# Performance work log

Measured on AMD Instinct MI355X. Metric: run time of the kernel, lower is better.

Reference implementation:

```python
import jax, jax.numpy as jnp
import numpy as np

BOX_WARP = 1.2
BMIN, BMAX = -0.6, 0.6   # sampler bbox
EPS_FD = 0.01            # finite-difference eps for SDF normals
RADIUS = 0.5             # sphere sdf bias radius
INV_S = 80.0             # sdf -> density sharpness (softplus clamp mode)
S_PER_RAY = 96


def _grid_sample_one(feat, uv):
    # feat: [C,H,W]; uv: [M,2] in [-1,1]; bilinear, align_corners=False, zeros padding
    C, H, W = feat.shape
    x = ((uv[:, 0] + 1.0) * W - 1.0) * 0.5
    y = ((uv[:, 1] + 1.0) * H - 1.0) * 0.5
    x0 = jnp.floor(x).astype(jnp.int32)
    y0 = jnp.floor(y).astype(jnp.int32)
    wx = x - x0
    wy = y - y0

    def g(ix, iy):
        valid = ((ix >= 0) & (ix < W) & (iy >= 0) & (iy < H)).astype(feat.dtype)
        v = feat[:, jnp.clip(iy, 0, H - 1), jnp.clip(ix, 0, W - 1)]  # [C,M]
        return v * valid[None, :]

    out = (g(x0, y0) * (1 - wx) * (1 - wy) + g(x0 + 1, y0) * wx * (1 - wy)
           + g(x0, y0 + 1) * (1 - wx) * wy + g(x0 + 1, y0 + 1) * wx * wy)
    return out.T  # [M,C]


def sample_from_planes(planes, coords):
    # planes: [N,3,C,H,W]; coords: [N,M,3] -> [N,M,3*C]
    N, P, C, H, W = planes.shape
    M = coords.shape[1]
    nc = coords * (2.0 / BOX_WARP)
    proj = jnp.stack([nc[..., (0, 1)], nc[..., (0, 2)], nc[..., (1, 2)]], axis=1)  # [N,3,M,2]
    s = jax.vmap(_grid_sample_one)(planes.reshape(N * P, C, H, W), proj.reshape(N * P, M, 2))
    return s.reshape(N, P, M, C).transpose(0, 2, 1, 3).reshape(N, M, P * C)


def decode(planes, coords, W1, b1, W2, b2):
    x = sample_from_planes(planes, coords)
    return jax.nn.relu(x @ W1 + b1) @ W2 + b2  # [N,M,4]


def render(planes, ro, rd, W1, b1, W2, b2):
    N, R, _ = ro.shape
    S = S_PER_RAY
    safe_rd = jnp.where(jnp.abs(rd) < 1e-9, 1e-9, rd)
    t1 = (BMIN - ro) / safe_rd
    t2 = (BMAX - ro) / safe_rd
    tn = jnp.maximum(jnp.max(jnp.minimum(t1, t2), axis=-1), 0.0)   # [N,R] ray_start (auto box)
    tf = jnp.min(jnp.maximum(t1, t2), axis=-1)                      # [N,R] ray_end
    span = jnp.maximum(tf - tn, 0.0)
    frac = (jnp.arange(S, dtype=ro.dtype) + 0.5) / S
    depths = tn[..., None] + span[..., None] * frac                 # [N,R,S]
    pts = (ro[:, :, None, :] + depths[..., None] * rd[:, :, None, :]).reshape(N, R * S, 3)

    x = decode(planes, pts, W1, b1, W2, b2)
    sdf = x[..., 0:1]
    rgb = jax.nn.sigmoid(x[..., 1:]) * (1 + 2 * 0.001) - 0.001

    # finite-difference SDF gradient (3 extra decoder passes)
    eye = jnp.eye(3, dtype=pts.dtype) * EPS_FD
    sdf_off = jnp.stack(
        [decode(planes, jnp.clip(pts + eye[i], BMIN, BMAX), W1, b1, W2, b2)[..., 0] for i in range(3)],
        axis=-1)                                                    # [N,M,3]
    sdf_grad = (sdf_off - sdf) / EPS_FD
    normal = sdf_grad / (jnp.linalg.norm(sdf_grad, axis=-1, keepdims=True) + 1e-8)

    # sphere sdf bias, sdf -> density, alpha compositing
    shifted = sdf[..., 0] + (jnp.linalg.norm(pts, axis=-1) - RADIUS)
    sigma = jax.nn.softplus(-shifted * INV_S).reshape(N, R, S)
    delta = (span / S)[..., None]
    alpha = 1.0 - jnp.exp(-sigma * delta)
    T = jnp.cumprod(1.0 - alpha + 1e-10, axis=-1)
    T = jnp.concatenate([jnp.ones_like(T[..., :1]), T[..., :-1]], axis=-1)
    w = alpha * T                                                   # [N,R,S]

    rgb_s = (w[..., None] * rgb.reshape(N, R, S, 3)).sum(-2)
    wsum = w.sum(-1, keepdims=True)
    rgb_s = rgb_s + (1.0 - wsum)                                    # white background
    depth_s = (w * depths).sum(-1, keepdims=True)
    normal_s = (w[..., None] * normal.reshape(N, R, S, 3)).sum(-2)
    return rgb_s, depth_s, wsum, sdf_grad, normal_s


def reference(planes, ray_origins, ray_directions, W1, b1, W2, b2, render_size):
    N = planes.shape[0]
    rgb_s, depth_s, wsum, sdf_grad, normal_s = render(planes, ray_origins, ray_directions, W1, b1, W2, b2)
    n = normal_s / (jnp.linalg.norm(normal_s, axis=-1, keepdims=True) + 1e-8)
    n = (n + 1.0) * 0.5
    n = n * wsum  # lerp(0, n, opacity)
    H = W = render_size
    comp_rgb = rgb_s.transpose(0, 2, 1).reshape(N, 3, H, W)
    comp_depth = depth_s.transpose(0, 2, 1).reshape(N, 1, H, W)
    opacity = wsum.transpose(0, 2, 1).reshape(N, 1, H, W)
    comp_normal = n.transpose(0, 2, 1).reshape(N, 3, H, W)
    return (comp_rgb, comp_depth, opacity, comp_normal, sdf_grad)


def setup_inputs():
    key = jax.random.key(0)
    k0, k1, k2 = jax.random.split(key, 3)
    N, C, Hp, rs = 1, 80, 64, 64
    planes = jax.random.normal(k0, (N, 3, C, Hp, Hp), jnp.float32)
    u = jnp.linspace(-0.45, 0.45, rs)
    uu, vv = jnp.meshgrid(u, u, indexing='xy')
    d = jnp.stack([uu, vv, -jnp.ones_like(uu)], -1).reshape(-1, 3)
    d = d / jnp.linalg.norm(d, axis=-1, keepdims=True)
    ray_directions = jnp.broadcast_to(d, (N, rs * rs, 3)).astype(jnp.float32)
    ray_origins = jnp.broadcast_to(jnp.array([0.0, 0.0, 1.5], jnp.float32), (N, rs * rs, 3))
    W1 = jax.random.normal(k1, (3 * C, 64), jnp.float32) * 0.05
    b1 = jnp.zeros((64,), jnp.float32)
    W2 = jax.random.normal(k2, (64, 4), jnp.float32) * 0.05
    b2 = jnp.zeros((4,), jnp.float32)
    return {"planes": planes, "ray_origins": ray_origins, "ray_directions": ray_directions,
            "W1": W1, "b1": b1, "W2": W2, "b2": b2, "render_size": rs}
```

## Files before the change

### kernel.cpp

```cpp
#include <hip/hip_runtime.h>
#include <hip/hip_bf16.h>
#include <hip/hip_fp16.h>

#define NUM_RAYS 4096
#define S_PER 96
#define NPTS (NUM_RAYS * S_PER)
#define CCH 80
#define HID 64

#define WSB_W2     256
#define WSB_B1     1536
#define WSB_B2     1856
#define WSB_W1S    4096
#define WSB_PT     40960



typedef __attribute__((ext_vector_type(8))) _Float16 half8;
typedef __attribute__((ext_vector_type(4))) float f32x4;

__device__ __forceinline__ float bf2f(__hip_bfloat16 v) { return __bfloat162float(v); }

__device__ __forceinline__ short f2hs(float f) {
  __half h = __float2half(f);
  short s; __builtin_memcpy(&s, &h, 2); return s;
}

template <bool BF16>
__device__ __forceinline__ float ldin(const void* p, size_t i) {
  if (BF16) return bf2f(((const __hip_bfloat16*)p)[i]);
  else      return ((const float*)p)[i];
}
template <bool BF16>
__device__ __forceinline__ void stout(void* p, size_t i, float v) {
  if (BF16) ((__hip_bfloat16*)p)[i] = __float2bfloat16(v);
  else      ((float*)p)[i] = v;
}

__device__ __forceinline__ __half2 h2cast(unsigned u) {
  __half2 r; __builtin_memcpy(&r, &u, 4); return r;
}

__device__ __forceinline__ bool detect_bf16(const void* rdv) {
  int lane = threadIdx.x & 63;
  const __hip_bfloat16* p = (const __hip_bfloat16*)rdv;
  float x = bf2f(p[lane * 3 + 0]);
  float y = bf2f(p[lane * 3 + 1]);
  float z = bf2f(p[lane * 3 + 2]);
  float n2 = x * x + y * y + z * z;
  bool ok = (n2 > 0.95f) && (n2 < 1.05f);
  return __ballot(ok) == ~0ull;
}

template <bool BF16>
__device__ __forceinline__ void prep_body(const void* __restrict__ W1,
                                          const void* __restrict__ b1,
                                          const void* __restrict__ W2,
                                          const void* __restrict__ b2,
                                          float* __restrict__ ws, int tid) {
  unsigned short* w1sw = (unsigned short*)((char*)ws + WSB_W1S);
  if (tid < 15360) {
    int p = tid / 5120;
    int r = tid - p * 5120;
    int ch, n;
    if (r < 4096) {
      int ccl  = r >> 11;
      int r2   = r & 2047;
      int j    = r2 & 7;
      int lane = (r2 >> 3) & 63;
      int nb   = r2 >> 9;
      ch = ccl * 32 + 8 * (lane >> 4) + j;
      n  = nb * 16 + (lane & 15);
    } else {
      int r2   = r - 4096;
      int j    = r2 & 7;
      int l31  = (r2 >> 3) & 31;
      int nb   = r2 >> 8;
      ch = 64 + 8 * (l31 >> 4) + j;
      n  = nb * 16 + (l31 & 15);
    }
    w1sw[tid] = (unsigned short)f2hs(ldin<BF16>(W1, (size_t)(p * 80 + ch) * 64 + n));
  }
  float* w2f = (float*)((char*)ws + WSB_W2);
  float* b1f = (float*)((char*)ws + WSB_B1);
  float* b2f = (float*)((char*)ws + WSB_B2);
  if (tid < 256) w2f[tid] = ldin<BF16>(W2, tid);
  if (tid < 64)  b1f[tid] = ldin<BF16>(b1, tid);
  if (tid < 4)   b2f[tid] = ldin<BF16>(b2, tid);
}

template <bool BF16>
__device__ __forceinline__ void transpose_body(const void* __restrict__ planes,
                                               float* __restrict__ ws) {
  int b  = blockIdx.x;
  int tt = b & 15;
  int ct = (b >> 4) % 5;
  int p  = b / 80;
  int tex = tt * 256 + threadIdx.x;
  unsigned u[8];
  #pragma unroll
  for (int i = 0; i < 8; i++) {
    int c0 = ct * 16 + 2 * i;
    float v0 = ldin<BF16>(planes, ((size_t)(p * 80 + c0) * 4096) + tex);
    float v1 = ldin<BF16>(planes, ((size_t)(p * 80 + c0 + 1) * 4096) + tex);
    unsigned s0 = (unsigned short)f2hs(v0);
    unsigned s1 = (unsigned short)f2hs(v1);
    u[i] = s0 | (s1 << 16);
  }
  unsigned short* ptb = (unsigned short*)((char*)ws + WSB_PT);
  uint4* dst = (uint4*)(ptb + ((size_t)(p * 4096 + tex) * 80 + ct * 16));
  dst[0] = make_uint4(u[0], u[1], u[2], u[3]);
  dst[1] = make_uint4(u[4], u[5], u[6], u[7]);
}

__global__ void setup_kernel(const void* __restrict__ planes,
                             const void* __restrict__ W1,
                             const void* __restrict__ b1,
                             const void* __restrict__ W2,
                             const void* __restrict__ b2,
                             const void* __restrict__ rd,
                             float* __restrict__ ws) {
  bool bf = detect_bf16(rd);
  if (blockIdx.x < 240) {
    if (bf) transpose_body<true >(planes, ws);
    else    transpose_body<false>(planes, ws);
  } else {
    int tid = (blockIdx.x - 240) * 256 + threadIdx.x;
    if (bf) prep_body<true >(W1, b1, W2, b2, ws, tid);
    else    prep_body<false>(W1, b1, W2, b2, ws, tid);
  }
}

struct TapInfo {
  float w00, w10, w01, w11;
  int o00, o10, o01, o11;
};
__device__ __forceinline__ TapInfo tap_setup(float u, float v) {
  TapInfo t;
  float fx = u * 32.0f + 31.5f;
  float fy = v * 32.0f + 31.5f;
  float flx = floorf(fx), fly = floorf(fy);
  int x0 = (int)flx, y0 = (int)fly;
  float wx = fx - flx, wy = fy - fly;
  int x1 = x0 + 1, y1 = y0 + 1;
  bool vx0 = (x0 >= 0) && (x0 < 64);
  bool vx1 = (x1 >= 0) && (x1 < 64);
  bool vy0 = (y0 >= 0) && (y0 < 64);
  bool vy1 = (y1 >= 0) && (y1 < 64);
  int cx0 = min(max(x0, 0), 63), cx1 = min(max(x1, 0), 63);
  int cy0 = min(max(y0, 0), 63), cy1 = min(max(y1, 0), 63);
  t.w00 = (1.0f - wx) * (1.0f - wy) * ((vx0 && vy0) ? 1.0f : 0.0f);
  t.w10 = wx * (1.0f - wy)          * ((vx1 && vy0) ? 1.0f : 0.0f);
  t.w01 = (1.0f - wx) * wy          * ((vx0 && vy1) ? 1.0f : 0.0f);
  t.w11 = wx * wy                   * ((vx1 && vy1) ? 1.0f : 0.0f);
  t.o00 = cy0 * 64 + cx0; t.o10 = cy0 * 64 + cx1;
  t.o01 = cy1 * 64 + cx0; t.o11 = cy1 * 64 + cx1;
  return t;
}

template <bool BF16>
__device__ __forceinline__ void fused_body(const void* __restrict__ ro,
                                           const void* __restrict__ rd,
                                           const float* __restrict__ ws,
                                           void* __restrict__ out,
                                           unsigned short* __restrict__ w1s,
                                           float* __restrict__ rec_v0,
                                           __half (*__restrict__ rec_h)[6],
                                           float* __restrict__ xfer,
                                           float (*__restrict__ red)[8]) {
  const unsigned short* ptb = (const unsigned short*)((const char*)ws + WSB_PT);
  const float* w2f = (const float*)((const char*)ws + WSB_W2);
  const float* b1f = (const float*)((const char*)ws + WSB_B1);
  const float* b2f = (const float*)((const char*)ws + WSB_B2);

  int tid = threadIdx.x;
  int wave = tid >> 6;
  int lane = tid & 63;
  int lane15 = lane & 15;
  int quad = lane >> 4;
  int ray = blockIdx.x;

  {
    const uint4* src = (const uint4*)((const char*)ws + WSB_W1S);
    uint4* dst = (uint4*)w1s;
    #pragma unroll
    for (int t = 0; t < 8; t++) {
      int idx = tid + 256 * t;
      if (idx < 1920) dst[idx] = src[idx];
    }
  }
  float4 w2reg[4];
  #pragma unroll
  for (int nb = 0; nb < 4; nb++)
    w2reg[nb] = *(const float4*)(w2f + (nb * 16 + lane15) * 4);

  float ox = ldin<BF16>(ro, (size_t)ray*3+0), oy = ldin<BF16>(ro, (size_t)ray*3+1), oz = ldin<BF16>(ro, (size_t)ray*3+2);
  float dx = ldin<BF16>(rd, (size_t)ray*3+0), dy = ldin<BF16>(rd, (size_t)ray*3+1), dz = ldin<BF16>(rd, (size_t)ray*3+2);
  float o3[3] = {ox, oy, oz}, d3[3] = {dx, dy, dz};
  float tmin = -1e30f, tmax = 1e30f;
  #pragma unroll
  for (int k = 0; k < 3; k++) {
    float sd = (fabsf(d3[k]) < 1e-9f) ? 1e-9f : d3[k];
    float ta = (-0.6f - o3[k]) / sd;
    float tb = ( 0.6f - o3[k]) / sd;
    tmin = fmaxf(tmin, fminf(ta, tb));
    tmax = fminf(tmax, fmaxf(ta, tb));
  }
  float tn = fmaxf(tmin, 0.0f);
  float span = fmaxf(tmax - tn, 0.0f);
  float delta = span * (1.0f / (float)S_PER);
  float b1x[4];
  #pragma unroll
  for (int nb = 0; nb < 4; nb++) b1x[nb] = b1f[nb * 16 + lane15];

  __syncthreads();

  #pragma unroll 1
  for (int it = 0; it < 6; it++) {
    int sbase = it * 16 + wave * 4;

    int sF = sbase + (lane15 >> 2);
    int d  = lane15 & 3;
    float depF = tn + span * (((float)sF + 0.5f) * (1.0f / (float)S_PER));
    float px = ox + depF * dx, py = oy + depF * dy, pz = oz + depF * dz;
    if (d == 1) px += 0.01f;
    if (d == 2) py += 0.01f;
    if (d == 3) pz += 0.01f;
    if (d > 0) {
      px = fminf(fmaxf(px, -0.6f), 0.6f);
      py = fminf(fmaxf(py, -0.6f), 0.6f);
      pz = fminf(fmaxf(pz, -0.6f), 0.6f);
    }
    const float inv = 1.0f / 0.6f;
    float ux = px * inv, uy = py * inv, uz = pz * inv;

    f32x4 acc[4];
    #pragma unroll
    for (int nb = 0; nb < 4; nb++) acc[nb] = (f32x4){0.f, 0.f, 0.f, 0.f};

    #pragma unroll 1
    for (int p = 0; p < 3; p++) {
      float u = (p == 2) ? uy : ux;
      float v = (p == 0) ? uy : uz;
      TapInfo t = tap_setup(u, v);
      __half2 hw00 = __float2half2_rn(t.w00);
      __half2 hw10 = __float2half2_rn(t.w10);
      __half2 hw01 = __float2half2_rn(t.w01);
      __half2 hw11 = __float2half2_rn(t.w11);
      const unsigned short* c00p = ptb + (size_t)p * 327680 + t.o00 * 80 + 8 * quad;
      const unsigned short* c10p = ptb + (size_t)p * 327680 + t.o10 * 80 + 8 * quad;
      const unsigned short* c01p = ptb + (size_t)p * 327680 + t.o01 * 80 + 8 * quad;
      const unsigned short* c11p = ptb + (size_t)p * 327680 + t.o11 * 80 + 8 * quad;
      const unsigned short* w1p = w1s + p * 5120;
      #pragma unroll
      for (int ccl = 0; ccl < 3; ccl++) {
        int4 afi = {0, 0, 0, 0};
        if (ccl < 2 || quad < 2) {
          uint4 q00 = *(const uint4*)(c00p + 32 * ccl);
          uint4 q10 = *(const uint4*)(c10p + 32 * ccl);
          uint4 q01 = *(const uint4*)(c01p + 32 * ccl);
          uint4 q11 = *(const uint4*)(c11p + 32 * ccl);
          unsigned u00[4] = {q00.x, q00.y, q00.z, q00.w};
          unsigned u10[4] = {q10.x, q10.y, q10.z, q10.w};
          unsigned u01[4] = {q01.x, q01.y, q01.z, q01.w};
          unsigned u11[4] = {q11.x, q11.y, q11.z, q11.w};
          int ae[4];
          #pragma unroll
          for (int q = 0; q < 4; q++) {
            __half2 f = __hmul2(h2cast(u00[q]), hw00);
            f = __hfma2(h2cast(u10[q]), hw10, f);
            f = __hfma2(h2cast(u01[q]), hw01, f);
            f = __hfma2(h2cast(u11[q]), hw11, f);
            int fi; __builtin_memcpy(&fi, &f, 4);
            ae[q] = fi;
          }
          afi.x = ae[0]; afi.y = ae[1]; afi.z = ae[2]; afi.w = ae[3];
        }
        half8 afr;
        __builtin_memcpy(&afr, &afi, 16);
        #pragma unroll
        for (int nb = 0; nb < 4; nb++) {
          int boff = (ccl < 2) ? (ccl * 2048 + (nb * 64 + lane) * 8)
                               : (4096 + (nb * 32 + (lane & 31)) * 8);
          half8 bfr = *(const half8*)(w1p + boff);
          acc[nb] = __builtin_amdgcn_mfma_f32_16x16x32_f16(afr, bfr, acc[nb], 0, 0, 0);
        }
      }
    }

    float vals[7];
    #pragma unroll
    for (int k = 0; k < 7; k++) vals[k] = 0.0f;
    #pragma unroll
    for (int nb = 0; nb < 4; nb++) {
      float4 w2r = w2reg[nb];
      float hr0 = fmaxf(acc[nb][0] + b1x[nb], 0.0f);
      vals[0] = fmaf(hr0, w2r.x, vals[0]);
      vals[4] = fmaf(hr0, w2r.y, vals[4]);
      vals[5] = fmaf(hr0, w2r.z, vals[5]);
      vals[6] = fmaf(hr0, w2r.w, vals[6]);
      float hr1 = fmaxf(acc[nb][1] + b1x[nb], 0.0f);
      float hr2 = fmaxf(acc[nb][2] + b1x[nb], 0.0f);
      float hr3 = fmaxf(acc[nb][3] + b1x[nb], 0.0f);
      vals[1] = fmaf(hr1, w2r.x, vals[1]);
      vals[2] = fmaf(hr2, w2r.x, vals[2]);
      vals[3] = fmaf(hr3, w2r.x, vals[3]);
    }
    #pragma unroll
    for (int mask = 1; mask < 16; mask <<= 1) {
      #pragma unroll
      for (int k = 0; k < 7; k++) vals[k] += __shfl_xor(vals[k], mask, 64);
    }

    if (lane15 == 0) {
      int sE = sbase + quad;
      rec_v0[sE] = vals[0];
      rec_h[sE][0] = __float2half(vals[1] - vals[0]);
      rec_h[sE][1] = __float2half(vals[2] - vals[0]);
      rec_h[sE][2] = __float2half(vals[3] - vals[0]);
      rec_h[sE][3] = __float2half(vals[4]);
      rec_h[sE][4] = __float2half(vals[5]);
      rec_h[sE][5] = __float2half(vals[6]);
    }
  }

  __syncthreads();

  float b2_0 = b2f[0], b2_1 = b2f[1], b2_2 = b2f[2], b2_3 = b2f[3];
  float a = 0.f, l = 0.f, pcr = 0.f, pcg = 0.f, pcb = 0.f, pnx = 0.f, pny = 0.f, pnz = 0.f, pdt = 0.f;
  if (tid < S_PER) {
    float v0 = rec_v0[tid];
    float d1 = __half2float(rec_h[tid][0]);
    float d2 = __half2float(rec_h[tid][1]);
    float d3 = __half2float(rec_h[tid][2]);
    float v4 = __half2float(rec_h[tid][3]);
    float v5 = __half2float(rec_h[tid][4]);
    float v6 = __half2float(rec_h[tid][5]);
    float sdf0 = v0 + b2_0;
    float g0 = d1 * 100.0f;
    float g1 = d2 * 100.0f;
    float g2 = d3 * 100.0f;
    size_t gid = (size_t)ray * S_PER + tid;
    stout<BF16>(out, (size_t)32768 + gid * 3 + 0, g0);
    stout<BF16>(out, (size_t)32768 + gid * 3 + 1, g1);
    stout<BF16>(out, (size_t)32768 + gid * 3 + 2, g2);
    pcr = 1.0f / (1.0f + expf(-(v4 + b2_1))) * 1.002f - 0.001f;
    pcg = 1.0f / (1.0f + expf(-(v5 + b2_2))) * 1.002f - 0.001f;
    pcb = 1.0f / (1.0f + expf(-(v6 + b2_3))) * 1.002f - 0.001f;
    pdt = tn + span * (((float)tid + 0.5f) * (1.0f / (float)S_PER));
    float ex = ox + pdt * dx, ey = oy + pdt * dy, ez = oz + pdt * dz;
    float pn = sqrtf(ex * ex + ey * ey + ez * ez);
    float shifted = sdf0 + pn - 0.5f;
    float xarg = -shifted * 80.0f;
    float sigma = (xarg > 20.0f) ? xarg : log1pf(expf(xarg));
    a = 1.0f - expf(-sigma * delta);
    float gl = sqrtf(g0 * g0 + g1 * g1 + g2 * g2) + 1e-8f;
    float igl = 1.0f / gl;
    pnx = g0 * igl; pny = g1 * igl; pnz = g2 * igl;
    l = logf(1.0f - a + 1e-10f);
  }

  float lv = l;
  #pragma unroll
  for (int off = 1; off < 64; off <<= 1) {
    float up = __shfl_up(lv, off, 64);
    if (lane >= off) lv += up;
  }
  if (tid == 63) xfer[0] = lv;
  __syncthreads();
  if (tid >= 64 && tid < S_PER) lv += xfer[0];

  float T = expf(lv - l);
  float w = (tid < S_PER) ? a * T : 0.0f;
  float q[8];
  q[0] = w;
  q[1] = w * pcr; q[2] = w * pcg; q[3] = w * pcb;
  q[4] = w * pnx; q[5] = w * pny; q[6] = w * pnz;
  q[7] = w * pdt;
  #pragma unroll
  for (int off = 1; off < 64; off <<= 1) {
    #pragma unroll
    for (int k = 0; k < 8; k++) q[k] += __shfl_xor(q[k], off, 64);
  }
  if (lane == 0) {
    #pragma unroll
    for (int k = 0; k < 8; k++) red[wave][k] = q[k];
  }
  __syncthreads();
  if (tid == 0) {
    float R[8];
    #pragma unroll
    for (int k = 0; k < 8; k++) R[k] = red[0][k] + red[1][k] + red[2][k] + red[3][k];
    float wsum = R[0];
    float nl = sqrtf(R[4] * R[4] + R[5] * R[5] + R[6] * R[6]) + 1e-8f;
    float inl = 1.0f / nl;
    float nrm3[3] = {R[4], R[5], R[6]};
    float rgb3[3] = {R[1], R[2], R[3]};
    #pragma unroll
    for (int c = 0; c < 3; c++) {
      float n = (nrm3[c] * inl + 1.0f) * 0.5f * wsum;
      stout<BF16>(out, (size_t)(c * 4096 + ray), rgb3[c] + 1.0f - wsum);
      stout<BF16>(out, (size_t)(20480 + c * 4096 + ray), n);
    }
    stout<BF16>(out, (size_t)(12288 + ray), R[7]);
    stout<BF16>(out, (size_t)(16384 + ray), wsum);
  }
}

__global__ __launch_bounds__(256) void fused_kernel(
    const void* __restrict__ ro,
    const void* __restrict__ rd,
    const float* __restrict__ ws,
    void* __restrict__ out) {
  __shared__ __align__(16) unsigned short w1s[15360];
  __shared__ float rec_v0[S_PER];
  __shared__ __half rec_h[S_PER][6];
  __shared__ float xfer[1];
  __shared__ float red[4][8];

  if (detect_bf16(rd)) fused_body<true >(ro, rd, ws, out, w1s, rec_v0, rec_h, xfer, red);
  else                 fused_body<false>(ro, rd, ws, out, w1s, rec_v0, rec_h, xfer, red);
}

extern "C" void kernel_launch(void* const* d_in, const int* in_sizes, int n_in,
                              void* d_out, int out_size, void* d_ws, size_t ws_size,
                              hipStream_t stream) {
  const void* planes = d_in[0];
  const void* ro     = d_in[1];
  const void* rd     = d_in[2];
  const void* W1     = d_in[3];
  const void* b1     = d_in[4];
  const void* W2     = d_in[5];
  const void* b2     = d_in[6];
  float* ws = (float*)d_ws;

  setup_kernel<<<304, 256, 0, stream>>>(planes, W1, b1, W2, b2, rd, ws);
  fused_kernel<<<NUM_RAYS, 256, 0, stream>>>(ro, rd, ws, d_out);
}
```

Measured before the change: 247.3 us.

## Unroll plane loop with double-buffered tap loads, DPP row reductions, W2 in LDS

Fully unrolls the three-plane loop and precomputes all bilinear tap offsets and weights up front. The four-corner feature loads for the next chunk are issued while the current chunk is blended and fed to MFMA, using two alternating register buffers. The goal is to hide global/L2 gather latency behind the f16 blending and matrix math. The 16-lane reduction now uses DPP row rotations instead of shfl_xor, and W2 moves from per-thread registers to shared memory to offset the extra registers the pipeline holds. The added live registers could lower occupancy.

```diff
diff --git a/kernel.cpp b/kernel.cpp
--- a/kernel.cpp
+++ b/kernel.cpp
@@ -40,6 +40,13 @@
 __device__ __forceinline__ __half2 h2cast(unsigned u) {
   __half2 r; __builtin_memcpy(&r, &u, 4); return r;
 }
+
+#define DPP_ADD(V, CTRL)                                                     \
+  do {                                                                       \
+    int s_ = __float_as_int(V);                                              \
+    int t_ = __builtin_amdgcn_update_dpp(0, s_, (CTRL), 0xF, 0xF, true);     \
+    V += __int_as_float(t_);                                                 \
+  } while (0)
 
 __device__ __forceinline__ bool detect_bf16(const void* rdv) {
   int lane = threadIdx.x & 63;
@@ -164,6 +171,7 @@
                                            const float* __restrict__ ws,
                                            void* __restrict__ out,
                                            unsigned short* __restrict__ w1s,
+                                           float* __restrict__ w2s,
                                            float* __restrict__ rec_v0,
                                            __half (*__restrict__ rec_h)[6],
                                            float* __restrict__ xfer,
@@ -189,10 +197,7 @@
       if (idx < 1920) dst[idx] = src[idx];
     }
   }
-  float4 w2reg[4];
-  #pragma unroll
-  for (int nb = 0; nb < 4; nb++)
-    w2reg[nb] = *(const float4*)(w2f + (nb * 16 + lane15) * 4);
+  w2s[tid] = w2f[tid];
 
   float ox = ldin<BF16>(ro, (size_t)ray*3+0), oy = ldin<BF16>(ro, (size_t)ray*3+1), oz = ldin<BF16>(ro, (size_t)ray*3+2);
   float dx = ldin<BF16>(rd, (size_t)ray*3+0), dy = ldin<BF16>(rd, (size_t)ray*3+1), dz = ldin<BF16>(rd, (size_t)ray*3+2);
@@ -215,6 +220,8 @@
 
   __syncthreads();
 
+  const char* pb = (const char*)ptb + 16 * quad;
+
   #pragma unroll 1
   for (int it = 0; it < 6; it++) {
     int sbase = it * 16 + wave * 4;
@@ -234,66 +241,94 @@
     const float inv = 1.0f / 0.6f;
     float ux = px * inv, uy = py * inv, uz = pz * inv;
 
+    TapInfo t0 = tap_setup(ux, uy);
+    TapInfo t1 = tap_setup(ux, uz);
+    TapInfo t2 = tap_setup(uy, uz);
+    unsigned f000 = (unsigned)(t0.o00 * 160);
+    unsigned f010 = (unsigned)(t0.o10 * 160);
+    unsigned f001 = (unsigned)(t0.o01 * 160);
+    unsigned f011 = (unsigned)(t0.o11 * 160);
+    unsigned f100 = (unsigned)(t1.o00 * 160) + 655360u;
+    unsigned f110 = (unsigned)(t1.o10 * 160) + 655360u;
+    unsigned f101 = (unsigned)(t1.o01 * 160) + 655360u;
+    unsigned f111 = (unsigned)(t1.o11 * 160) + 655360u;
+    unsigned f200 = (unsigned)(t2.o00 * 160) + 1310720u;
+    unsigned f210 = (unsigned)(t2.o10 * 160) + 1310720u;
+    unsigned f201 = (unsigned)(t2.o01 * 160) + 1310720u;
+    unsigned f211 = (unsigned)(t2.o11 * 160) + 1310720u;
+    __half2 h000 = __float2half2_rn(t0.w00), h010 = __float2half2_rn(t0.w10);
+    __half2 h001 = __float2half2_rn(t0.w01), h011 = __float2half2_rn(t0.w11);
+    __half2 h100 = __float2half2_rn(t1.w00), h110 = __float2half2_rn(t1.w10);
+    __half2 h101 = __float2half2_rn(t1.w01), h111 = __float2half2_rn(t1.w11);
+    __half2 h200 = __float2half2_rn(t2.w00), h210 = __float2half2_rn(t2.w10);
+    __half2 h201 = __float2half2_rn(t2.w01), h211 = __float2half2_rn(t2.w11);
+
     f32x4 acc[4];
     #pragma unroll
     for (int nb = 0; nb < 4; nb++) acc[nb] = (f32x4){0.f, 0.f, 0.f, 0.f};
 
-    #pragma unroll 1
-    for (int p = 0; p < 3; p++) {
-      float u = (p == 2) ? uy : ux;
-      float v = (p == 0) ? uy : uz;
-      TapInfo t = tap_setup(u, v);
-      __half2 hw00 = __float2half2_rn(t.w00);
-      __half2 hw10 = __float2half2_rn(t.w10);
-      __half2 hw01 = __float2half2_rn(t.w01);
-      __half2 hw11 = __float2half2_rn(t.w11);
-      const unsigned short* c00p = ptb + (size_t)p * 327680 + t.o00 * 80 + 8 * quad;
-      const unsigned short* c10p = ptb + (size_t)p * 327680 + t.o10 * 80 + 8 * quad;
-      const unsigned short* c01p = ptb + (size_t)p * 327680 + t.o01 * 80 + 8 * quad;
-      const unsigned short* c11p = ptb + (size_t)p * 327680 + t.o11 * 80 + 8 * quad;
-      const unsigned short* w1p = w1s + p * 5120;
-      #pragma unroll
-      for (int ccl = 0; ccl < 3; ccl++) {
-        int4 afi = {0, 0, 0, 0};
-        if (ccl < 2 || quad < 2) {
-          uint4 q00 = *(const uint4*)(c00p + 32 * ccl);
-          uint4 q10 = *(const uint4*)(c10p + 32 * ccl);
-          uint4 q01 = *(const uint4*)(c01p + 32 * ccl);
-          uint4 q11 = *(const uint4*)(c11p + 32 * ccl);
-          unsigned u00[4] = {q00.x, q00.y, q00.z, q00.w};
-          unsigned u10[4] = {q10.x, q10.y, q10.z, q10.w};
-          unsigned u01[4] = {q01.x, q01.y, q01.z, q01.w};
-          unsigned u11[4] = {q11.x, q11.y, q11.z, q11.w};
-          int ae[4];
-          #pragma unroll
-          for (int q = 0; q < 4; q++) {
-            __half2 f = __hmul2(h2cast(u00[q]), hw00);
-            f = __hfma2(h2cast(u10[q]), hw10, f);
-            f = __hfma2(h2cast(u01[q]), hw01, f);
-            f = __hfma2(h2cast(u11[q]), hw11, f);
-            int fi; __builtin_memcpy(&fi, &f, 4);
-            ae[q] = fi;
-          }
-          afi.x = ae[0]; afi.y = ae[1]; afi.z = ae[2]; afi.w = ae[3];
-        }
-        half8 afr;
-        __builtin_memcpy(&afr, &afi, 16);
-        #pragma unroll
-        for (int nb = 0; nb < 4; nb++) {
-          int boff = (ccl < 2) ? (ccl * 2048 + (nb * 64 + lane) * 8)
-                               : (4096 + (nb * 32 + (lane & 31)) * 8);
-          half8 bfr = *(const half8*)(w1p + boff);
-          acc[nb] = __builtin_amdgcn_mfma_f32_16x16x32_f16(afr, bfr, acc[nb], 0, 0, 0);
-        }
-      }
-    }
+    uint4 A0, A1, A2, A3, B0, B1, B2, B3;
+
+#define LOADT(D0, D1, D2, D3, O00, O10, O01, O11, CCL)                        \
+    do {                                                                      \
+      if ((CCL) < 2 || quad < 2) {                                            \
+        D0 = *(const uint4*)(pb + O00 + 64 * (CCL));                          \
+        D1 = *(const uint4*)(pb + O10 + 64 * (CCL));                          \
+        D2 = *(const uint4*)(pb + O01 + 64 * (CCL));                          \
+        D3 = *(const uint4*)(pb + O11 + 64 * (CCL));                          \
+      }                                                                       \
+    } while (0)
+
+#define BLENDT(S0, S1, S2, S3, W00, W10, W01, W11, P, CCL)                    \
+    do {                                                                      \
+      int4 afi = {0, 0, 0, 0};                                                \
+      if ((CCL) < 2 || quad < 2) {                                            \
+        unsigned u00_[4] = {S0.x, S0.y, S0.z, S0.w};                          \
+        unsigned u10_[4] = {S1.x, S1.y, S1.z, S1.w};                          \
+        unsigned u01_[4] = {S2.x, S2.y, S2.z, S2.w};                          \
+        unsigned u11_[4] = {S3.x, S3.y, S3.z, S3.w};                          \
+        int ae_[4];                                                           \
+        _Pragma("unroll")                                                     \
+        for (int q = 0; q < 4; q++) {                                         \
+          __half2 f = __hmul2(h2cast(u00_[q]), W00);                          \
+          f = __hfma2(h2cast(u10_[q]), W10, f);                               \
+          f = __hfma2(h2cast(u01_[q]), W01, f);                               \
+          f = __hfma2(h2cast(u11_[q]), W11, f);                               \
+          int fi_; __builtin_memcpy(&fi_, &f, 4);                             \
+          ae_[q] = fi_;                                                       \
+        }                                                                     \
+        afi.x = ae_[0]; afi.y = ae_[1]; afi.z = ae_[2]; afi.w = ae_[3];       \
+      }                                                                       \
+      half8 afr;                                                              \
+      __builtin_memcpy(&afr, &afi, 16);                                       \
+      _Pragma("unroll")                                                       \
+      for (int nb = 0; nb < 4; nb++) {                                        \
+        int boff = ((CCL) < 2) ? ((CCL) * 2048 + (nb * 64 + lane) * 8)        \
+                               : (4096 + (nb * 32 + (lane & 31)) * 8);        \
+        half8 bfr = *(const half8*)(w1s + (P) * 5120 + boff);                 \
+        acc[nb] = __builtin_amdgcn_mfma_f32_16x16x32_f16(afr, bfr, acc[nb], 0, 0, 0); \
+      }                                                                       \
+    } while (0)
+
+    LOADT(A0, A1, A2, A3, f000, f010, f001, f011, 0);
+    LOADT(B0, B1, B2, B3, f000, f010, f001, f011, 1);  BLENDT(A0, A1, A2, A3, h000, h010, h001, h011, 0, 0);
+    LOADT(A0, A1, A2, A3, f000, f010, f001, f011, 2);  BLENDT(B0, B1, B2, B3, h000, h010, h001, h011, 0, 1);
+    LOADT(B0, B1, B2, B3, f100, f110, f101, f111, 0);  BLENDT(A0, A1, A2, A3, h000, h010, h001, h011, 0, 2);
+    LOADT(A0, A1, A2, A3, f100, f110, f101, f111, 1);  BLENDT(B0, B1, B2, B3, h100, h110, h101, h111, 1, 0);
+    LOADT(B0, B1, B2, B3, f100, f110, f101, f111, 2);  BLENDT(A0, A1, A2, A3, h100, h110, h101, h111, 1, 1);
+    LOADT(A0, A1, A2, A3, f200, f210, f201, f211, 0);  BLENDT(B0, B1, B2, B3, h100, h110, h101, h111, 1, 2);
+    LOADT(B0, B1, B2, B3, f200, f210, f201, f211, 1);  BLENDT(A0, A1, A2, A3, h200, h210, h201, h211, 2, 0);
+    LOADT(A0, A1, A2, A3, f200, f210, f201, f211, 2);  BLENDT(B0, B1, B2, B3, h200, h210, h201, h211, 2, 1);
+                                                       BLENDT(A0, A1, A2, A3, h200, h210, h201, h211, 2, 2);
+#undef LOADT
+#undef BLENDT
 
     float vals[7];
     #pragma unroll
     for (int k = 0; k < 7; k++) vals[k] = 0.0f;
     #pragma unroll
     for (int nb = 0; nb < 4; nb++) {
-      float4 w2r = w2reg[nb];
+      float4 w2r = *(const float4*)(w2s + (nb * 16 + lane15) * 4);
       float hr0 = fmaxf(acc[nb][0] + b1x[nb], 0.0f);
       vals[0] = fmaf(hr0, w2r.x, vals[0]);
       vals[4] = fmaf(hr0, w2r.y, vals[4]);
@@ -307,9 +342,11 @@
       vals[3] = fmaf(hr3, w2r.x, vals[3]);
     }
     #pragma unroll
-    for (int mask = 1; mask < 16; mask <<= 1) {
-      #pragma unroll
-      for (int k = 0; k < 7; k++) vals[k] += __shfl_xor(vals[k], mask, 64);
+    for (int k = 0; k < 7; k++) {
+      DPP_ADD(vals[k], 0x121);
+      DPP_ADD(vals[k], 0x122);
+      DPP_ADD(vals[k], 0x124);
+      DPP_ADD(vals[k], 0x128);
     }
 
     if (lane15 == 0) {
@@ -413,13 +450,14 @@
     const float* __restrict__ ws,
     void* __restrict__ out) {
   __shared__ __align__(16) unsigned short w1s[15360];
+  __shared__ float w2s[256];
   __shared__ float rec_v0[S_PER];
   __shared__ __half rec_h[S_PER][6];
   __shared__ float xfer[1];
   __shared__ float red[4][8];
 
-  if (detect_bf16(rd)) fused_body<true >(ro, rd, ws, out, w1s, rec_v0, rec_h, xfer, red);
-  else                 fused_body<false>(ro, rd, ws, out, w1s, rec_v0, rec_h, xfer, red);
+  if (detect_bf16(rd)) fused_body<true >(ro, rd, ws, out, w1s, w2s, rec_v0, rec_h, xfer, red);
+  else                 fused_body<false>(ro, rd, ws, out, w1s, w2s, rec_v0, rec_h, xfer, red);
 }
 
 extern "C" void kernel_launch(void* const* d_in, const int* in_sizes, int n_in,
```

Measured after the change: 343.1 us. 38.7% more time.
